# Performance work log

Measured on AMD Instinct MI355X. Metric: run time of the kernel, lower is better.

The kernel has to match this reference:

```python
import jax, jax.numpy as jnp
import numpy as np

N = 50000      # nodes
E = 1600000    # edges
IN_DIM = 128
HID = 32
OUT = 32
HEADS = 4
NEG_SLOPE = 0.2  # DGL GATConv default leaky_relu slope


def setup_inputs() -> dict:
    key = jax.random.key(0)
    ks = jax.random.split(key, 16)
    h = jax.random.normal(ks[0], (N, IN_DIM), dtype=jnp.float32)
    src = jax.random.randint(ks[1], (E,), 0, N, dtype=jnp.int32)
    dst = jax.random.randint(ks[2], (E,), 0, N, dtype=jnp.int32)
    s = 0.1
    # layer 1: in_dim -> (HEADS, HID)
    W1 = jax.random.normal(ks[3], (IN_DIM, HEADS * HID), dtype=jnp.float32) * s
    al1 = jax.random.normal(ks[4], (HEADS, HID), dtype=jnp.float32) * s
    ar1 = jax.random.normal(ks[5], (HEADS, HID), dtype=jnp.float32) * s
    b1 = jnp.zeros((HEADS * HID,), dtype=jnp.float32)
    # layer 2: HEADS*HID -> (HEADS, HID)
    W2 = jax.random.normal(ks[6], (HEADS * HID, HEADS * HID), dtype=jnp.float32) * s
    al2 = jax.random.normal(ks[7], (HEADS, HID), dtype=jnp.float32) * s
    ar2 = jax.random.normal(ks[8], (HEADS, HID), dtype=jnp.float32) * s
    b2 = jnp.zeros((HEADS * HID,), dtype=jnp.float32)
    # layer 3: HEADS*HID -> (HEADS, OUT)
    W3 = jax.random.normal(ks[9], (HEADS * HID, HEADS * OUT), dtype=jnp.float32) * s
    al3 = jax.random.normal(ks[10], (HEADS, OUT), dtype=jnp.float32) * s
    ar3 = jax.random.normal(ks[11], (HEADS, OUT), dtype=jnp.float32) * s
    b3 = jnp.zeros((HEADS * OUT,), dtype=jnp.float32)
    return {"h": h, "src": src, "dst": dst,
            "W1": W1, "al1": al1, "ar1": ar1, "b1": b1,
            "W2": W2, "al2": al2, "ar2": ar2, "b2": b2,
            "W3": W3, "al3": al3, "ar3": ar3, "b3": b3}


def gat_layer(h, W, al, ar, b, src, dst):
    """DGL-style GATConv. h:[N,F] -> [N,H,D]."""
    H, D = al.shape
    ft = (h @ W).reshape(-1, H, D)                      # [N,H,D]
    el = jnp.einsum('nhd,hd->nh', ft, al)               # [N,H]
    er = jnp.einsum('nhd,hd->nh', ft, ar)               # [N,H]
    e = jax.nn.leaky_relu(el[src] + er[dst], NEG_SLOPE)  # [E,H]
    # edge softmax grouped by destination node
    m = jax.ops.segment_max(e, dst, num_segments=N)     # [N,H]
    ex = jnp.exp(e - m[dst])
    z = jax.ops.segment_sum(ex, dst, num_segments=N)    # [N,H]
    a = ex / z[dst]                                     # [E,H]
    msg = ft[src] * a[:, :, None]                       # [E,H,D]
    rst = jax.ops.segment_sum(msg, dst, num_segments=N)  # [N,H,D]
    return rst + b.reshape(1, H, D)


def reference(h, src, dst, W1, al1, ar1, b1, W2, al2, ar2, b2, W3, al3, ar3, b3):
    x = gat_layer(h, W1, al1, ar1, b1, src, dst).reshape(N, -1)  # flatten(1)
    x = jax.nn.elu(x)  # dropout is identity at eval
    x = gat_layer(x, W2, al2, ar2, b2, src, dst).reshape(N, -1)
    x = jax.nn.elu(x)
    x = gat_layer(x, W3, al3, ar3, b3, src, dst).mean(axis=1)    # [N,OUT]
    return x
```

## Files before the change

### kernel.cpp

```cpp
#include <hip/hip_runtime.h>
#include <hip/hip_fp16.h>

#define NEG_SLOPE 0.2f
#define C1   2048
#define BKT  196
#define BSTR 9216

__device__ __forceinline__ unsigned int encf(float f) {
    unsigned int u = __float_as_uint(f);
    return (u & 0x80000000u) ? ~u : (u | 0x80000000u);
}
__device__ __forceinline__ float decf(unsigned int u) {
    return (u & 0x80000000u) ? __uint_as_float(u & 0x7fffffffu)
                             : __uint_as_float(~u);
}

__global__ __launch_bounds__(256) void gemm128(const float* __restrict__ X,
    const float* __restrict__ W, const float* __restrict__ al,
    const float* __restrict__ ar, __half* __restrict__ C16,
    float* __restrict__ el, float* __restrict__ er,
    unsigned int* __restrict__ maxbuf, int M)
{
    __shared__ float Xs[32][68];
    __shared__ float Ws[32][128];
    __shared__ unsigned int lmax[8];
    const int t    = threadIdx.x;
    const int row0 = blockIdx.x * 64;
    const int rg   = t >> 5;
    const int cg   = t & 31;
    float acc[8][4];
#pragma unroll
    for (int i = 0; i < 8; ++i) { acc[i][0]=0.f; acc[i][1]=0.f; acc[i][2]=0.f; acc[i][3]=0.f; }
    if (t < 8) lmax[t] = 0;

    for (int kc = 0; kc < 4; ++kc) {
        const int k0 = kc * 32;
        {
            const int lr = t >> 2;
            const int lk = (t & 3) * 8;
            int gr = row0 + lr; if (gr >= M) gr = M - 1;
            const float4* s4 = (const float4*)&X[(size_t)gr * 128 + k0 + lk];
            float4 a = s4[0], b = s4[1];
            Xs[lk+0][lr]=a.x; Xs[lk+1][lr]=a.y; Xs[lk+2][lr]=a.z; Xs[lk+3][lr]=a.w;
            Xs[lk+4][lr]=b.x; Xs[lk+5][lr]=b.y; Xs[lk+6][lr]=b.z; Xs[lk+7][lr]=b.w;
        }
        {
            const int lk = t >> 3;
            const int lc = (t & 7) * 16;
            const float4* s4 = (const float4*)&W[(size_t)(k0 + lk) * 128 + lc];
            float4* dd = (float4*)&Ws[lk][lc];
            dd[0]=s4[0]; dd[1]=s4[1]; dd[2]=s4[2]; dd[3]=s4[3];
        }
        __syncthreads();
#pragma unroll
        for (int k = 0; k < 32; ++k) {
            float4 wv = *(const float4*)&Ws[k][cg * 4];
            float4 x0 = *(const float4*)&Xs[k][rg * 8];
            float4 x1 = *(const float4*)&Xs[k][rg * 8 + 4];
            float xr[8] = {x0.x,x0.y,x0.z,x0.w,x1.x,x1.y,x1.z,x1.w};
#pragma unroll
            for (int i = 0; i < 8; ++i) {
                acc[i][0] += xr[i] * wv.x;
                acc[i][1] += xr[i] * wv.y;
                acc[i][2] += xr[i] * wv.z;
                acc[i][3] += xr[i] * wv.w;
            }
        }
        __syncthreads();
    }
#pragma unroll
    for (int i = 0; i < 8; ++i) {
        int gr = row0 + rg * 8 + i;
        if (gr < M) {
            __half2 h0 = __floats2half2_rn(acc[i][0], acc[i][1]);
            __half2 h1 = __floats2half2_rn(acc[i][2], acc[i][3]);
            uint2 pv;
            pv.x = __builtin_bit_cast(unsigned int, h0);
            pv.y = __builtin_bit_cast(unsigned int, h1);
            *(uint2*)&C16[(size_t)gr * 128 + cg * 4] = pv;
        }
    }
    {
        const float4 alv = *(const float4*)&al[cg * 4];
        const float4 arv = *(const float4*)&ar[cg * 4];
        float pl[8], pr[8];
#pragma unroll
        for (int i = 0; i < 8; ++i) {
            pl[i] = acc[i][0]*alv.x + acc[i][1]*alv.y + acc[i][2]*alv.z + acc[i][3]*alv.w;
            pr[i] = acc[i][0]*arv.x + acc[i][1]*arv.y + acc[i][2]*arv.z + acc[i][3]*arv.w;
        }
#pragma unroll
        for (int off = 1; off < 8; off <<= 1) {
#pragma unroll
            for (int i = 0; i < 8; ++i) {
                pl[i] += __shfl_xor(pl[i], off);
                pr[i] += __shfl_xor(pr[i], off);
            }
        }
        if ((cg & 7) == 0) {
            const int head = cg >> 3;
            float plm = pl[0], prm = pr[0];
#pragma unroll
            for (int i = 1; i < 8; ++i) { plm = fmaxf(plm, pl[i]); prm = fmaxf(prm, pr[i]); }
            atomicMax(&lmax[head], encf(plm));
            atomicMax(&lmax[4 + head], encf(prm));
#pragma unroll
            for (int i = 0; i < 8; ++i) {
                int gr = row0 + rg * 8 + i;
                if (gr < M) {
                    el[(size_t)gr * 4 + head] = pl[i];
                    er[(size_t)gr * 4 + head] = pr[i];
                }
            }
        }
        __syncthreads();
        if (t < 8) atomicMax(&maxbuf[t], lmax[t]);
    }
}

__global__ __launch_bounds__(256) void p1_bucket(const int* __restrict__ src,
    const int* __restrict__ dst, unsigned int* __restrict__ tmp,
    unsigned int* __restrict__ bcnt, int E_)
{
    __shared__ unsigned int hist[256];
    __shared__ unsigned int sc[256];
    __shared__ unsigned int ebase[256];
    __shared__ unsigned int gbase[256];
    __shared__ unsigned int buf[C1];
    const int t  = threadIdx.x;
    const int e0 = blockIdx.x * C1;
    hist[t] = 0;
    __syncthreads();
    int  s_[8], d_[8];
    bool v_[8];
#pragma unroll
    for (int k = 0; k < 2; ++k) {
        int idx = e0 + k * 1024 + t * 4;
        if (idx + 3 < E_) {
            int4 sv = *(const int4*)&src[idx];
            int4 dv = *(const int4*)&dst[idx];
            s_[k*4+0]=sv.x; s_[k*4+1]=sv.y; s_[k*4+2]=sv.z; s_[k*4+3]=sv.w;
            d_[k*4+0]=dv.x; d_[k*4+1]=dv.y; d_[k*4+2]=dv.z; d_[k*4+3]=dv.w;
            v_[k*4+0]=true; v_[k*4+1]=true; v_[k*4+2]=true; v_[k*4+3]=true;
        } else {
            for (int j = 0; j < 4; ++j) {
                int e = idx + j;
                v_[k*4+j] = e < E_;
                s_[k*4+j] = v_[k*4+j] ? src[e] : 0;
                d_[k*4+j] = v_[k*4+j] ? dst[e] : 0;
            }
        }
    }
#pragma unroll
    for (int j = 0; j < 8; ++j) if (v_[j]) atomicAdd(&hist[d_[j] >> 8], 1u);
    __syncthreads();
    const unsigned int cnt_t = hist[t];
    sc[t] = cnt_t;
    __syncthreads();
    for (int off = 1; off < 256; off <<= 1) {
        unsigned int v = (t >= off) ? sc[t - off] : 0;
        __syncthreads();
        sc[t] += v;
        __syncthreads();
    }
    const unsigned int excl = sc[t] - cnt_t;
    ebase[t] = excl;
    gbase[t] = (t < BKT && cnt_t > 0) ? atomicAdd(&bcnt[t], cnt_t) : 0u;
    hist[t] = excl;
    __syncthreads();
#pragma unroll
    for (int j = 0; j < 8; ++j) {
        if (v_[j]) {
            int b = d_[j] >> 8;
            unsigned int pos = atomicAdd(&hist[b], 1u);
            buf[pos] = ((unsigned int)s_[j] << 8) | (unsigned int)(d_[j] & 255);
        }
    }
    __syncthreads();
    const int total = min(C1, E_ - e0);
    for (int i = t; i < total; i += 256) {
        int lo = 0, hi = 255;
        while (lo < hi) { int mid = (lo + hi) >> 1; if (sc[mid] > (unsigned int)i) hi = mid; else lo = mid + 1; }
        unsigned int off = gbase[lo] + ((unsigned int)i - ebase[lo]);
        if (off < BSTR) tmp[(size_t)lo * BSTR + off] = buf[i];
    }
}

__global__ __launch_bounds__(256) void scanB(const unsigned int* __restrict__ bcnt,
    unsigned int* __restrict__ bbase, unsigned int* __restrict__ maxinit, int E_)
{
    __shared__ unsigned int sc[256];
    const int t = threadIdx.x;
    const unsigned int v = (t < BKT) ? bcnt[t] : 0;
    sc[t] = v;
    __syncthreads();
    for (int off = 1; off < 256; off <<= 1) {
        unsigned int u = (t >= off) ? sc[t - off] : 0;
        __syncthreads();
        sc[t] += u;
        __syncthreads();
    }
    if (t < BKT) bbase[t] = sc[t] - v;
    if (t == BKT) bbase[t] = (unsigned int)E_;
    if (t < 24) maxinit[t] = 0;
}

__global__ __launch_bounds__(256) void p2_scatter(const unsigned int* __restrict__ tmp,
    const unsigned int* __restrict__ bcnt, const unsigned int* __restrict__ bbase,
    int* __restrict__ rowptr, int* __restrict__ esrc_s, int Nn)
{
    __shared__ unsigned int hist[256], sc[256], cur[256];
    __shared__ unsigned int ent[BSTR];
    const int t = threadIdx.x;
    const int b = blockIdx.x;
    const unsigned int cnt  = min(bcnt[b], (unsigned int)BSTR);
    const unsigned int base = bbase[b];
    hist[t] = 0;
    __syncthreads();
    for (unsigned int i = t; i < cnt; i += 256) {
        unsigned int e = tmp[(size_t)b * BSTR + i];
        ent[i] = e;
        atomicAdd(&hist[e & 255u], 1u);
    }
    __syncthreads();
    const unsigned int c_t = hist[t];
    sc[t] = c_t;
    __syncthreads();
    for (int off = 1; off < 256; off <<= 1) {
        unsigned int u = (t >= off) ? sc[t - off] : 0;
        __syncthreads();
        sc[t] += u;
        __syncthreads();
    }
    const unsigned int excl = sc[t] - c_t;
    cur[t] = base + excl;
    const int n = (b << 8) + t;
    if (n <= Nn) rowptr[n] = (int)(base + excl);
    __syncthreads();
    for (unsigned int i = t; i < cnt; i += 256) {
        unsigned int e = ent[i];
        unsigned int p = atomicAdd(&cur[e & 255u], 1u);
        esrc_s[p] = (int)(e >> 8);
    }
}

template <int MODE>
__global__ __launch_bounds__(256) void attn_agg(
    const __half* __restrict__ ft, const float* __restrict__ el,
    const float* __restrict__ er, const int* __restrict__ rowptr,
    const int* __restrict__ esrc, const float* __restrict__ bias,
    const unsigned int* __restrict__ mbuf, float* __restrict__ out, int Nn)
{
    const int t = threadIdx.x;
    const int l = t & 63;
    const int n = blockIdx.x * 4 + (t >> 6);
    if (n >= Nn) return;
    const int g    = l >> 4;
    const int q    = l & 15;
    const int head = q >> 2;

    const int start = rowptr[n];
    const int end   = rowptr[n + 1];
    const bool any  = end > start;

    const float er_h = er[(size_t)n * 4 + head];
    const float msum = decf(mbuf[head]) + decf(mbuf[4 + head]);
    const float mh   = msum > 0.f ? msum : NEG_SLOPE * msum;

    const uint4* __restrict__ ftq = (const uint4*)ft;

    float acc[8];
#pragma unroll
    for (int j = 0; j < 8; ++j) acc[j] = 0.f;
    float z = 0.f;

    const int c0   = start & ~3;
    const int last = end - 1;

    int  sA = 0, sB = 0, sC = 0;
    uint4 fA = make_uint4(0,0,0,0), fB;
    float eA = 0.f, eB;

    if (any) {
        int e0i = c0 + g;       e0i = e0i < start ? start : (e0i > last ? last : e0i);
        int e1i = c0 + 4 + g;   e1i = e1i < start ? start : (e1i > last ? last : e1i);
        sA = esrc[e0i];
        sB = esrc[e1i];
        fA = ftq[(size_t)sA * 16 + q];
        eA = el[(size_t)sA * 4 + head];
    }

    for (int c = c0; c < end; c += 4) {
        {
            int e2 = c + 8 + g;
            e2 = e2 < start ? start : (e2 > last ? last : e2);
            sC = esrc[e2];
        }
        fB = ftq[(size_t)sB * 16 + q];
        eB = el[(size_t)sB * 4 + head];
        {
            const int e = c + g;
            float x = eA + er_h;
            x = fmaxf(x, NEG_SLOPE * x);
            const float ex = (e >= start && e < end) ? __expf(x - mh) : 0.f;
            z += ex;
            const float2 f0 = __half22float2(__builtin_bit_cast(__half2, fA.x));
            const float2 f1 = __half22float2(__builtin_bit_cast(__half2, fA.y));
            const float2 f2 = __half22float2(__builtin_bit_cast(__half2, fA.z));
            const float2 f3 = __half22float2(__builtin_bit_cast(__half2, fA.w));
            acc[0] += ex * f0.x; acc[1] += ex * f0.y;
            acc[2] += ex * f1.x; acc[3] += ex * f1.y;
            acc[4] += ex * f2.x; acc[5] += ex * f2.y;
            acc[6] += ex * f3.x; acc[7] += ex * f3.y;
        }
        sA = sB; sB = sC; fA = fB; eA = eB;
    }

#pragma unroll
    for (int j = 0; j < 8; ++j) {
        acc[j] += __shfl_xor(acc[j], 16);
        acc[j] += __shfl_xor(acc[j], 32);
    }
    z += __shfl_xor(z, 16);
    z += __shfl_xor(z, 32);

    const float inv = any ? 1.f / z : 0.f;

    if (MODE == 0) {
        if (l < 32) {
            float r0, r1, r2, r3;
            if (l < 16) { r0 = acc[0]; r1 = acc[1]; r2 = acc[2]; r3 = acc[3]; }
            else        { r0 = acc[4]; r1 = acc[5]; r2 = acc[6]; r3 = acc[7]; }
            const int f0 = 8 * q + 4 * (l >> 4);
            const float4 b4 = *(const float4*)&bias[f0];
            float vx = r0 * inv + b4.x;
            float vy = r1 * inv + b4.y;
            float vz = r2 * inv + b4.z;
            float vw = r3 * inv + b4.w;
            vx = vx > 0.f ? vx : __expf(vx) - 1.f;
            vy = vy > 0.f ? vy : __expf(vy) - 1.f;
            vz = vz > 0.f ? vz : __expf(vz) - 1.f;
            vw = vw > 0.f ? vw : __expf(vw) - 1.f;
            *(float4*)&out[(size_t)n * 128 + f0] = make_float4(vx, vy, vz, vw);
        }
    } else {
        float v[8];
        const float4 ba = *(const float4*)&bias[8 * q];
        const float4 bb = *(const float4*)&bias[8 * q + 4];
        v[0] = acc[0] * inv + ba.x; v[1] = acc[1] * inv + ba.y;
        v[2] = acc[2] * inv + ba.z; v[3] = acc[3] * inv + ba.w;
        v[4] = acc[4] * inv + bb.x; v[5] = acc[5] * inv + bb.y;
        v[6] = acc[6] * inv + bb.z; v[7] = acc[7] * inv + bb.w;
#pragma unroll
        for (int j = 0; j < 8; ++j) {
            v[j] += __shfl_xor(v[j], 4);
            v[j] += __shfl_xor(v[j], 8);
        }
        if (l < 4) {
            *(float4*)&out[(size_t)n * 32 + 8 * q] =
                make_float4(0.25f * v[0], 0.25f * v[1], 0.25f * v[2], 0.25f * v[3]);
            *(float4*)&out[(size_t)n * 32 + 8 * q + 4] =
                make_float4(0.25f * v[4], 0.25f * v[5], 0.25f * v[6], 0.25f * v[7]);
        }
    }
}

extern "C" void kernel_launch(void* const* d_in, const int* in_sizes, int n_in,
                              void* d_out, int out_size, void* d_ws, size_t ws_size,
                              hipStream_t stream)
{
    const float* h   = (const float*)d_in[0];
    const int*   src = (const int*)d_in[1];
    const int*   dst = (const int*)d_in[2];
    const float* W1  = (const float*)d_in[3];
    const float* al1 = (const float*)d_in[4];
    const float* ar1 = (const float*)d_in[5];
    const float* b1  = (const float*)d_in[6];
    const float* W2  = (const float*)d_in[7];
    const float* al2 = (const float*)d_in[8];
    const float* ar2 = (const float*)d_in[9];
    const float* b2  = (const float*)d_in[10];
    const float* W3  = (const float*)d_in[11];
    const float* al3 = (const float*)d_in[12];
    const float* ar3 = (const float*)d_in[13];
    const float* b3  = (const float*)d_in[14];

    const int N = in_sizes[0] / 128;
    const int E = in_sizes[1];

    char* p = (char*)d_ws;
    auto alloc = [&](size_t bytes) {
        void* r = (void*)p;
        p += (bytes + 255) & ~(size_t)255;
        return r;
    };
    __half* ft    = (__half*)alloc((size_t)N * 128 * 4);
    float* xA     = (float*)alloc((size_t)N * 128 * 4);
    float* elbuf  = (float*)alloc((size_t)N * 4 * 4);
    float* erbuf  = (float*)alloc((size_t)N * 4 * 4);
    int*   rowptr = (int*)alloc((size_t)(N + 1) * 4);
    int*   esrc_s = (int*)alloc((size_t)E * 4);
    unsigned int* bcnt   = (unsigned int*)alloc((size_t)BKT * 4);
    unsigned int* bbase  = (unsigned int*)alloc((size_t)(BKT + 1) * 4);
    unsigned int* maxbuf = (unsigned int*)alloc(24 * 4);

    unsigned int* tmp = (unsigned int*)ft;

    const int NG4 = (N + 3) / 4;
    const int MG  = (N + 63) / 64;
    const int G1  = (E + C1 - 1) / C1;

    hipMemsetAsync(bcnt, 0, (size_t)BKT * 4, stream);
    p1_bucket<<<G1, 256, 0, stream>>>(src, dst, tmp, bcnt, E);
    scanB<<<1, 256, 0, stream>>>(bcnt, bbase, maxbuf, E);
    p2_scatter<<<BKT, 256, 0, stream>>>(tmp, bcnt, bbase, rowptr, esrc_s, N);

    gemm128<<<MG, 256, 0, stream>>>(h, W1, al1, ar1, ft, elbuf, erbuf, maxbuf, N);
    attn_agg<0><<<NG4, 256, 0, stream>>>(ft, elbuf, erbuf, rowptr, esrc_s, b1, maxbuf, xA, N);

    gemm128<<<MG, 256, 0, stream>>>(xA, W2, al2, ar2, ft, elbuf, erbuf, maxbuf + 8, N);
    attn_agg<0><<<NG4, 256, 0, stream>>>(ft, elbuf, erbuf, rowptr, esrc_s, b2, maxbuf + 8, xA, N);

    gemm128<<<MG, 256, 0, stream>>>(xA, W3, al3, ar3, ft, elbuf, erbuf, maxbuf + 16, N);
    attn_agg<1><<<NG4, 256, 0, stream>>>(ft, elbuf, erbuf, rowptr, esrc_s, b3, maxbuf + 16,
                                         (float*)d_out, N);
}
```

Measured before the change: 409.3 us.

## Enlarge GEMM register tile and use mixed-precision FMA in attention aggregation

The GEMM moves from 256 threads with 8x4 outputs each to 128 threads with 8x8 outputs each, and pads the W tile in shared memory. This raises arithmetic per shared-memory load but halves the threads per block. The attention aggregation loop gets a 2x manual unroll with ping-pong buffers, 32-bit byte-offset addressing, and inline v_fma_mix_f32 asm that multiplies fp16 features directly without separate conversions. The asm ties the code to the CDNA ISA, and the larger accumulator tile raises register pressure.

```diff
diff --git a/kernel.cpp b/kernel.cpp
--- a/kernel.cpp
+++ b/kernel.cpp
@@ -15,56 +15,66 @@
                              : __uint_as_float(~u);
 }
 
-__global__ __launch_bounds__(256) void gemm128(const float* __restrict__ X,
+#define FMA_MIX2(a0, a1, pk, s)                                               \
+    asm("v_fma_mix_f32 %0, %2, %3, %0 op_sel_hi:[1,0,0]\n\t"                  \
+        "v_fma_mix_f32 %1, %2, %3, %1 op_sel:[1,0,0] op_sel_hi:[1,0,0]"       \
+        : "+v"(a0), "+v"(a1) : "v"(pk), "v"(s))
+
+__global__ __launch_bounds__(128) void gemm128(const float* __restrict__ X,
     const float* __restrict__ W, const float* __restrict__ al,
     const float* __restrict__ ar, __half* __restrict__ C16,
     float* __restrict__ el, float* __restrict__ er,
     unsigned int* __restrict__ maxbuf, int M)
 {
     __shared__ float Xs[32][68];
-    __shared__ float Ws[32][128];
+    __shared__ float Ws[32][132];
     __shared__ unsigned int lmax[8];
     const int t    = threadIdx.x;
     const int row0 = blockIdx.x * 64;
-    const int rg   = t >> 5;
-    const int cg   = t & 31;
-    float acc[8][4];
-#pragma unroll
-    for (int i = 0; i < 8; ++i) { acc[i][0]=0.f; acc[i][1]=0.f; acc[i][2]=0.f; acc[i][3]=0.f; }
+    const int rg   = t >> 4;
+    const int cg   = t & 15;
+    float acc[8][8];
+#pragma unroll
+    for (int i = 0; i < 8; ++i)
+#pragma unroll
+        for (int j = 0; j < 8; ++j) acc[i][j] = 0.f;
     if (t < 8) lmax[t] = 0;
 
     for (int kc = 0; kc < 4; ++kc) {
         const int k0 = kc * 32;
         {
-            const int lr = t >> 2;
-            const int lk = (t & 3) * 8;
+            const int lr = t >> 1;
+            const int lk = (t & 1) * 16;
             int gr = row0 + lr; if (gr >= M) gr = M - 1;
             const float4* s4 = (const float4*)&X[(size_t)gr * 128 + k0 + lk];
-            float4 a = s4[0], b = s4[1];
-            Xs[lk+0][lr]=a.x; Xs[lk+1][lr]=a.y; Xs[lk+2][lr]=a.z; Xs[lk+3][lr]=a.w;
-            Xs[lk+4][lr]=b.x; Xs[lk+5][lr]=b.y; Xs[lk+6][lr]=b.z; Xs[lk+7][lr]=b.w;
+            float4 a = s4[0], b = s4[1], c = s4[2], d = s4[3];
+            Xs[lk+ 0][lr]=a.x; Xs[lk+ 1][lr]=a.y; Xs[lk+ 2][lr]=a.z; Xs[lk+ 3][lr]=a.w;
+            Xs[lk+ 4][lr]=b.x; Xs[lk+ 5][lr]=b.y; Xs[lk+ 6][lr]=b.z; Xs[lk+ 7][lr]=b.w;
+            Xs[lk+ 8][lr]=c.x; Xs[lk+ 9][lr]=c.y; Xs[lk+10][lr]=c.z; Xs[lk+11][lr]=c.w;
+            Xs[lk+12][lr]=d.x; Xs[lk+13][lr]=d.y; Xs[lk+14][lr]=d.z; Xs[lk+15][lr]=d.w;
         }
         {
-            const int lk = t >> 3;
-            const int lc = (t & 7) * 16;
-            const float4* s4 = (const float4*)&W[(size_t)(k0 + lk) * 128 + lc];
-            float4* dd = (float4*)&Ws[lk][lc];
-            dd[0]=s4[0]; dd[1]=s4[1]; dd[2]=s4[2]; dd[3]=s4[3];
+            const int kk = t >> 2;
+            const int cc = (t & 3) * 32;
+            const float4* s4 = (const float4*)&W[(size_t)(k0 + kk) * 128 + cc];
+            float4* dd = (float4*)&Ws[kk][cc];
+#pragma unroll
+            for (int j = 0; j < 8; ++j) dd[j] = s4[j];
         }
         __syncthreads();
 #pragma unroll
         for (int k = 0; k < 32; ++k) {
-            float4 wv = *(const float4*)&Ws[k][cg * 4];
+            float4 w0 = *(const float4*)&Ws[k][cg * 8];
+            float4 w1 = *(const float4*)&Ws[k][cg * 8 + 4];
             float4 x0 = *(const float4*)&Xs[k][rg * 8];
             float4 x1 = *(const float4*)&Xs[k][rg * 8 + 4];
             float xr[8] = {x0.x,x0.y,x0.z,x0.w,x1.x,x1.y,x1.z,x1.w};
-#pragma unroll
-            for (int i = 0; i < 8; ++i) {
-                acc[i][0] += xr[i] * wv.x;
-                acc[i][1] += xr[i] * wv.y;
-                acc[i][2] += xr[i] * wv.z;
-                acc[i][3] += xr[i] * wv.w;
-            }
+            float wc[8] = {w0.x,w0.y,w0.z,w0.w,w1.x,w1.y,w1.z,w1.w};
+#pragma unroll
+            for (int i = 0; i < 8; ++i)
+#pragma unroll
+                for (int j = 0; j < 8; ++j)
+                    acc[i][j] += xr[i] * wc[j];
         }
         __syncthreads();
     }
@@ -74,31 +84,40 @@
         if (gr < M) {
             __half2 h0 = __floats2half2_rn(acc[i][0], acc[i][1]);
             __half2 h1 = __floats2half2_rn(acc[i][2], acc[i][3]);
-            uint2 pv;
+            __half2 h2 = __floats2half2_rn(acc[i][4], acc[i][5]);
+            __half2 h3 = __floats2half2_rn(acc[i][6], acc[i][7]);
+            uint4 pv;
             pv.x = __builtin_bit_cast(unsigned int, h0);
             pv.y = __builtin_bit_cast(unsigned int, h1);
-            *(uint2*)&C16[(size_t)gr * 128 + cg * 4] = pv;
+            pv.z = __builtin_bit_cast(unsigned int, h2);
+            pv.w = __builtin_bit_cast(unsigned int, h3);
+            *(uint4*)&C16[(size_t)gr * 128 + cg * 8] = pv;
         }
     }
     {
-        const float4 alv = *(const float4*)&al[cg * 4];
-        const float4 arv = *(const float4*)&ar[cg * 4];
+        const int hcol = cg * 8;
+        const float4 al0 = *(const float4*)&al[hcol];
+        const float4 al1 = *(const float4*)&al[hcol + 4];
+        const float4 ar0 = *(const float4*)&ar[hcol];
+        const float4 ar1 = *(const float4*)&ar[hcol + 4];
         float pl[8], pr[8];
 #pragma unroll
         for (int i = 0; i < 8; ++i) {
-            pl[i] = acc[i][0]*alv.x + acc[i][1]*alv.y + acc[i][2]*alv.z + acc[i][3]*alv.w;
-            pr[i] = acc[i][0]*arv.x + acc[i][1]*arv.y + acc[i][2]*arv.z + acc[i][3]*arv.w;
-        }
-#pragma unroll
-        for (int off = 1; off < 8; off <<= 1) {
+            pl[i] = acc[i][0]*al0.x + acc[i][1]*al0.y + acc[i][2]*al0.z + acc[i][3]*al0.w
+                  + acc[i][4]*al1.x + acc[i][5]*al1.y + acc[i][6]*al1.z + acc[i][7]*al1.w;
+            pr[i] = acc[i][0]*ar0.x + acc[i][1]*ar0.y + acc[i][2]*ar0.z + acc[i][3]*ar0.w
+                  + acc[i][4]*ar1.x + acc[i][5]*ar1.y + acc[i][6]*ar1.z + acc[i][7]*ar1.w;
+        }
+#pragma unroll
+        for (int off = 1; off < 4; off <<= 1) {
 #pragma unroll
             for (int i = 0; i < 8; ++i) {
                 pl[i] += __shfl_xor(pl[i], off);
                 pr[i] += __shfl_xor(pr[i], off);
             }
         }
-        if ((cg & 7) == 0) {
-            const int head = cg >> 3;
+        if ((cg & 3) == 0) {
+            const int head = cg >> 2;
             float plm = pl[0], prm = pr[0];
 #pragma unroll
             for (int i = 1; i < 8; ++i) { plm = fmaxf(plm, pl[i]); prm = fmaxf(prm, pr[i]); }
@@ -267,53 +286,61 @@
     const float msum = decf(mbuf[head]) + decf(mbuf[4 + head]);
     const float mh   = msum > 0.f ? msum : NEG_SLOPE * msum;
 
-    const uint4* __restrict__ ftq = (const uint4*)ft;
+    const unsigned qo = (unsigned)(q * 16);
+    const unsigned ho = (unsigned)(head * 4);
 
     float acc[8];
 #pragma unroll
     for (int j = 0; j < 8; ++j) acc[j] = 0.f;
     float z = 0.f;
 
-    const int c0   = start & ~3;
-    const int last = end - 1;
-
-    int  sA = 0, sB = 0, sC = 0;
-    uint4 fA = make_uint4(0,0,0,0), fB;
-    float eA = 0.f, eB;
-
     if (any) {
-        int e0i = c0 + g;       e0i = e0i < start ? start : (e0i > last ? last : e0i);
-        int e1i = c0 + 4 + g;   e1i = e1i < start ? start : (e1i > last ? last : e1i);
-        sA = esrc[e0i];
-        sB = esrc[e1i];
-        fA = ftq[(size_t)sA * 16 + q];
-        eA = el[(size_t)sA * 4 + head];
-    }
-
-    for (int c = c0; c < end; c += 4) {
-        {
-            int e2 = c + 8 + g;
-            e2 = e2 < start ? start : (e2 > last ? last : e2);
-            sC = esrc[e2];
-        }
-        fB = ftq[(size_t)sB * 16 + q];
-        eB = el[(size_t)sB * 4 + head];
-        {
-            const int e = c + g;
-            float x = eA + er_h;
-            x = fmaxf(x, NEG_SLOPE * x);
-            const float ex = (e >= start && e < end) ? __expf(x - mh) : 0.f;
-            z += ex;
-            const float2 f0 = __half22float2(__builtin_bit_cast(__half2, fA.x));
-            const float2 f1 = __half22float2(__builtin_bit_cast(__half2, fA.y));
-            const float2 f2 = __half22float2(__builtin_bit_cast(__half2, fA.z));
-            const float2 f3 = __half22float2(__builtin_bit_cast(__half2, fA.w));
-            acc[0] += ex * f0.x; acc[1] += ex * f0.y;
-            acc[2] += ex * f1.x; acc[3] += ex * f1.y;
-            acc[4] += ex * f2.x; acc[5] += ex * f2.y;
-            acc[6] += ex * f3.x; acc[7] += ex * f3.y;
-        }
-        sA = sB; sB = sC; fA = fB; eA = eB;
+        const int c0   = start & ~3;
+        const int last = end - 1;
+        const int span = end - start;
+
+        auto clampi = [&](int e) -> int {
+            e = e < start ? start : e;
+            return e > last ? last : e;
+        };
+        auto ldft = [&](int s) -> uint4 {
+            return *(const uint4*)((const char*)ft + (((unsigned)s << 8) + qo));
+        };
+        auto ldel = [&](int s) -> float {
+            return *(const float*)((const char*)el + (((unsigned)s << 4) + ho));
+        };
+
+        int c = c0;
+        int sA = esrc[clampi(c + g)];
+        int sB = esrc[clampi(c + 4 + g)];
+        uint4 fA = ldft(sA), fB;
+        float eA = ldel(sA), eB;
+
+#define ATTN_COMPUTE(CC, F, EL)                                               \
+        {                                                                     \
+            const int eix = (CC) + g;                                         \
+            float x = (EL) + er_h;                                            \
+            x = fmaxf(x, NEG_SLOPE * x);                                      \
+            float ex = __expf(x - mh);                                        \
+            ex = ((unsigned)(eix - start) < (unsigned)span) ? ex : 0.f;       \
+            z += ex;                                                          \
+            FMA_MIX2(acc[0], acc[1], (F).x, ex);                              \
+            FMA_MIX2(acc[2], acc[3], (F).y, ex);                              \
+            FMA_MIX2(acc[4], acc[5], (F).z, ex);                              \
+            FMA_MIX2(acc[6], acc[7], (F).w, ex);                              \
+        }
+
+        while (true) {
+            sA = esrc[clampi(c + 8 + g)];
+            fB = ldft(sB); eB = ldel(sB);
+            ATTN_COMPUTE(c, fA, eA);
+            c += 4; if (c >= end) break;
+            sB = esrc[clampi(c + 8 + g)];
+            fA = ldft(sA); eA = ldel(sA);
+            ATTN_COMPUTE(c, fB, eB);
+            c += 4; if (c >= end) break;
+        }
+#undef ATTN_COMPUTE
     }
 
 #pragma unroll
@@ -415,13 +442,13 @@
     scanB<<<1, 256, 0, stream>>>(bcnt, bbase, maxbuf, E);
     p2_scatter<<<BKT, 256, 0, stream>>>(tmp, bcnt, bbase, rowptr, esrc_s, N);
 
-    gemm128<<<MG, 256, 0, stream>>>(h, W1, al1, ar1, ft, elbuf, erbuf, maxbuf, N);
+    gemm128<<<MG, 128, 0, stream>>>(h, W1, al1, ar1, ft, elbuf, erbuf, maxbuf, N);
     attn_agg<0><<<NG4, 256, 0, stream>>>(ft, elbuf, erbuf, rowptr, esrc_s, b1, maxbuf, xA, N);
 
-    gemm128<<<MG, 256, 0, stream>>>(xA, W2, al2, ar2, ft, elbuf, erbuf, maxbuf + 8, N);
+    gemm128<<<MG, 128, 0, stream>>>(xA, W2, al2, ar2, ft, elbuf, erbuf, maxbuf + 8, N);
     attn_agg<0><<<NG4, 256, 0, stream>>>(ft, elbuf, erbuf, rowptr, esrc_s, b2, maxbuf + 8, xA, N);
 
-    gemm128<<<MG, 256, 0, stream>>>(xA, W3, al3, ar3, ft, elbuf, erbuf, maxbuf + 16, N);
+    gemm128<<<MG, 128, 0, stream>>>(xA, W3, al3, ar3, ft, elbuf, erbuf, maxbuf + 16, N);
     attn_agg<1><<<NG4, 256, 0, stream>>>(ft, elbuf, erbuf, rowptr, esrc_s, b3, maxbuf + 16,
                                          (float*)d_out, N);
 }
```

After: 436.1 us. 6.5% more time.
